# Kernel optimization log

Hardware: AMD Instinct MI355X
Metric: run time of the kernel (lower is better)

The kernel has to match this reference:

```python
import jax, jax.numpy as jnp
import numpy as np

N_NODES = 50000
N_EDGES = 640000
D_IN = 128
D_HID = 128
D_OUT = 128


def setup_inputs() -> dict:
    key = jax.random.key(0)
    ks = jax.random.split(key, 8)
    x = jax.random.normal(ks[0], (N_NODES, D_IN), dtype=jnp.float32)
    edge_index = jax.random.randint(ks[1], (2, N_EDGES), 0, N_NODES, dtype=jnp.int64)
    s1 = 1.0 / np.sqrt(D_IN)
    s2 = 1.0 / np.sqrt(D_HID)
    W1_l = jax.random.uniform(ks[2], (D_IN, D_HID), jnp.float32, -s1, s1)
    W1_r = jax.random.uniform(ks[3], (D_IN, D_HID), jnp.float32, -s1, s1)
    b1 = jnp.zeros((D_HID,), jnp.float32)
    W2_l = jax.random.uniform(ks[4], (D_HID, D_OUT), jnp.float32, -s2, s2)
    W2_r = jax.random.uniform(ks[5], (D_HID, D_OUT), jnp.float32, -s2, s2)
    b2 = jnp.zeros((D_OUT,), jnp.float32)
    return {"x": x, "edge_index": edge_index,
            "W1_l": W1_l, "b1": b1, "W1_r": W1_r,
            "W2_l": W2_l, "b2": b2, "W2_r": W2_r}


def _sage_conv(x, src, dst, W_l, b_l, W_r, n_nodes):
    # mean-aggregate neighbor (source) features onto destinations
    agg = jax.ops.segment_sum(x[src], dst, num_segments=n_nodes)  # [N, d]
    cnt = jax.ops.segment_sum(jnp.ones((src.shape[0],), x.dtype), dst,
                              num_segments=n_nodes)  # [N]
    mean = agg / jnp.maximum(cnt, 1.0)[:, None]
    # PyG SAGEConv: lin_l(aggr) [with bias] + lin_r(x) [root weight, no bias]
    return mean @ W_l + b_l + x @ W_r


def reference(x, edge_index, W1_l, b1, W1_r, W2_l, b2, W2_r):
    src, dst = edge_index[0], edge_index[1]
    n = x.shape[0]
    h = _sage_conv(x, src, dst, W1_l, b1, W1_r, n)
    h = jax.nn.relu(h)
    h = _sage_conv(h, src, dst, W2_l, b2, W2_r, n)
    return h
```

## Files before the change

kernel.cpp:

```cpp
#include <hip/hip_runtime.h>

#define N_NODES 50000
#define N_EDGES 640000
#define D 128

#define SCAN_BLOCK 256
#define SCAN_NBLK ((N_NODES + SCAN_BLOCK - 1) / SCAN_BLOCK)

typedef __attribute__((ext_vector_type(8))) short bf16x8;
typedef __attribute__((ext_vector_type(4))) float f32x4;

__device__ __forceinline__ unsigned short f2bf(float f) {
    union { float f; unsigned u; } v; v.f = f;
    unsigned u = v.u;
    unsigned r = u + 0x7FFFu + ((u >> 16) & 1u);
    return (unsigned short)(r >> 16);
}
__device__ __forceinline__ float bf2f(unsigned short s) {
    union { unsigned u; float f; } v; v.u = ((unsigned)s) << 16; return v.f;
}

__global__ void deg_kernel(const int* __restrict__ dst, int* __restrict__ deg) {
    int e = blockIdx.x * blockDim.x + threadIdx.x;
    if (e < N_EDGES) atomicAdd(&deg[dst[e]], 1);
}

__global__ __launch_bounds__(SCAN_BLOCK) void scan_partial(const int* __restrict__ deg,
                                                           int* __restrict__ partial) {
    __shared__ int sm[SCAN_BLOCK];
    const int t = threadIdx.x;
    const int i = blockIdx.x * SCAN_BLOCK + t;
    sm[t] = (i < N_NODES) ? deg[i] : 0;
    __syncthreads();
#pragma unroll
    for (int off = SCAN_BLOCK / 2; off > 0; off >>= 1) {
        if (t < off) sm[t] += sm[t + off];
        __syncthreads();
    }
    if (t == 0) partial[blockIdx.x] = sm[0];
}

__global__ __launch_bounds__(SCAN_BLOCK) void scan_offsets(const int* __restrict__ partial,
                                                           int* __restrict__ block_off,
                                                           int* __restrict__ row_off) {
    __shared__ int sm[SCAN_BLOCK];
    const int t = threadIdx.x;
    int v = (t < SCAN_NBLK) ? partial[t] : 0;
    sm[t] = v;
    __syncthreads();
    int x = v;
#pragma unroll
    for (int off = 1; off < SCAN_BLOCK; off <<= 1) {
        int y = (t >= off) ? sm[t - off] : 0;
        __syncthreads();
        x += y;
        sm[t] = x;
        __syncthreads();
    }
    if (t < SCAN_NBLK) block_off[t] = x - v;
    if (t == SCAN_BLOCK - 1) row_off[N_NODES] = x;
}

__global__ __launch_bounds__(SCAN_BLOCK) void scan_final(const int* __restrict__ deg,
                                                         const int* __restrict__ block_off,
                                                         int* __restrict__ row_off,
                                                         int* __restrict__ cursor) {
    __shared__ int sm[SCAN_BLOCK];
    const int t = threadIdx.x;
    const int i = blockIdx.x * SCAN_BLOCK + t;
    int v = (i < N_NODES) ? deg[i] : 0;
    sm[t] = v;
    __syncthreads();
    int x = v;
#pragma unroll
    for (int off = 1; off < SCAN_BLOCK; off <<= 1) {
        int y = (t >= off) ? sm[t - off] : 0;
        __syncthreads();
        x += y;
        sm[t] = x;
        __syncthreads();
    }
    int excl = x - v + block_off[blockIdx.x];
    if (i < N_NODES) {
        row_off[i] = excl;
        cursor[i] = excl;
    }
}

__global__ void fill_csr(const int* __restrict__ src, const int* __restrict__ dst,
                         int* __restrict__ cursor, int* __restrict__ csr_src) {
    int e = blockIdx.x * blockDim.x + threadIdx.x;
    if (e < N_EDGES) {
        int pos = atomicAdd(&cursor[dst[e]], 1);
        csr_src[pos] = src[e];
    }
}

__global__ void cvt_and_wt(const float* __restrict__ x,
                           const float* __restrict__ W1l, const float* __restrict__ W1r,
                           const float* __restrict__ W2l, const float* __restrict__ W2r,
                           unsigned short* __restrict__ x_bf,
                           unsigned short* __restrict__ Wt1,
                           unsigned short* __restrict__ Wt2,
                           int* __restrict__ deg) {
    const int b = blockIdx.x;
    const int t = threadIdx.x;
    if (b < 3125) {
        int i = b * 256 + t;
        float4 a = *reinterpret_cast<const float4*>(&x[(size_t)i * 8]);
        float4 c = *reinterpret_cast<const float4*>(&x[(size_t)i * 8 + 4]);
        bf16x8 o;
        o[0] = (short)f2bf(a.x); o[1] = (short)f2bf(a.y);
        o[2] = (short)f2bf(a.z); o[3] = (short)f2bf(a.w);
        o[4] = (short)f2bf(c.x); o[5] = (short)f2bf(c.y);
        o[6] = (short)f2bf(c.z); o[7] = (short)f2bf(c.w);
        *reinterpret_cast<bf16x8*>(&x_bf[(size_t)i * 8]) = o;
    } else if (b < 3381) {
        const bool second = (b >= 3125 + 128);
        const float* Wl = second ? W2l : W1l;
        const float* Wr = second ? W2r : W1r;
        unsigned short* Wt = second ? Wt2 : Wt1;
        int i = (b - (second ? 3253 : 3125)) * 256 + t;
        int c = i >> 8, k = i & 255;
        float v = (k < 128) ? Wl[k * 128 + c] : Wr[(k - 128) * 128 + c];
        Wt[c * 256 + k] = f2bf(v);
    } else {
        int i = (b - 3381) * 256 + t;
        if (i < N_NODES) deg[i] = 0;
    }
}

template <bool RELU, bool OUTBF16>
__global__ __launch_bounds__(512) void sage_fused(
    const unsigned short* __restrict__ Aroot,
    const int* __restrict__ row_off,
    const int* __restrict__ csr_src,
    const unsigned short* __restrict__ Wt,
    const float* __restrict__ bias,
    float* __restrict__ outf,
    unsigned short* __restrict__ outb)
{
    __shared__ bf16x8 ws[4096];
    const int t = threadIdx.x;
    const int w = t >> 6;
    const int l = t & 63;
    const int row0 = blockIdx.x * 128 + w * 16;

    int node = row0 + (l & 15);
    if (node >= N_NODES) node = N_NODES - 1;
    const int k8 = (l >> 4) * 8;

#pragma unroll
    for (int i = 0; i < 8; ++i) {
        int g = i * 512 + t;
        int col = g >> 5;
        int chunk = g & 31;
        ws[col * 32 + (chunk ^ (col & 7))] =
            *reinterpret_cast<const bf16x8*>(&Wt[(size_t)g * 8]);
    }

    const int beg = row_off[node];
    const int end = row_off[node + 1];
    float s[4][8] = {};
    int k = beg;
    for (; k + 1 < end; k += 2) {
        int n0 = csr_src[k];
        int n1 = csr_src[k + 1];
        const unsigned short* b0 = &Aroot[(size_t)n0 * D + k8];
        const unsigned short* b1 = &Aroot[(size_t)n1 * D + k8];
        bf16x8 v0[4], v1[4];
#pragma unroll
        for (int kc = 0; kc < 4; ++kc)
            v0[kc] = *reinterpret_cast<const bf16x8*>(b0 + kc * 32);
#pragma unroll
        for (int kc = 0; kc < 4; ++kc)
            v1[kc] = *reinterpret_cast<const bf16x8*>(b1 + kc * 32);
#pragma unroll
        for (int kc = 0; kc < 4; ++kc)
#pragma unroll
            for (int j = 0; j < 8; ++j)
                s[kc][j] += bf2f((unsigned short)v0[kc][j])
                          + bf2f((unsigned short)v1[kc][j]);
    }
    if (k < end) {
        int n0 = csr_src[k];
        const unsigned short* b0 = &Aroot[(size_t)n0 * D + k8];
#pragma unroll
        for (int kc = 0; kc < 4; ++kc) {
            bf16x8 v0 = *reinterpret_cast<const bf16x8*>(b0 + kc * 32);
#pragma unroll
            for (int j = 0; j < 8; ++j) s[kc][j] += bf2f((unsigned short)v0[j]);
        }
    }

    bf16x8 a[8];
    {
        const float inv = 1.0f / fmaxf((float)(end - beg), 1.0f);
#pragma unroll
        for (int kc = 0; kc < 4; ++kc) {
            bf16x8 o;
#pragma unroll
            for (int j = 0; j < 8; ++j) o[j] = (short)f2bf(s[kc][j] * inv);
            a[kc] = o;
        }
    }
#pragma unroll
    for (int kc = 0; kc < 4; ++kc)
        a[4 + kc] = *reinterpret_cast<const bf16x8*>(
            &Aroot[(size_t)node * D + kc * 32 + k8]);

    __syncthreads();

    f32x4 acc[8] = {};
    const int l15 = l & 15;
    const int kg = l >> 4;
    const int swz = l & 7;
#pragma unroll
    for (int kc = 0; kc < 8; ++kc) {
#pragma unroll
        for (int c = 0; c < 8; ++c) {
            bf16x8 bfr = ws[c * 512 + l15 * 32 + ((kc * 4 + kg) ^ swz)];
            acc[c] = __builtin_amdgcn_mfma_f32_16x16x32_bf16(a[kc], bfr, acc[c], 0, 0, 0);
        }
    }

    const int rbase = row0 + kg * 4;
#pragma unroll
    for (int c = 0; c < 8; ++c) {
        const int col = c * 16 + l15;
        const float b = bias[col];
#pragma unroll
        for (int i = 0; i < 4; ++i) {
            int r = rbase + i;
            if (r < N_NODES) {
                float v = acc[c][i] + b;
                if (RELU) v = fmaxf(v, 0.f);
                if (OUTBF16) outb[(size_t)r * D + col] = f2bf(v);
                else         outf[(size_t)r * D + col] = v;
            }
        }
    }
}

extern "C" void kernel_launch(void* const* d_in, const int* in_sizes, int n_in,
                              void* d_out, int out_size, void* d_ws, size_t ws_size,
                              hipStream_t stream) {
    const float* x   = (const float*)d_in[0];
    const int*   ei  = (const int*)d_in[1];
    const float* W1l = (const float*)d_in[2];
    const float* b1  = (const float*)d_in[3];
    const float* W1r = (const float*)d_in[4];
    const float* W2l = (const float*)d_in[5];
    const float* b2  = (const float*)d_in[6];
    const float* W2r = (const float*)d_in[7];
    float* out = (float*)d_out;

    const int* src = ei;
    const int* dst = ei + N_EDGES;

    int* deg       = (int*)d_ws;
    int* row_off   = deg + 51200;
    int* cursor    = row_off + 51200;
    int* partial   = cursor + 51200;
    int* block_off = partial + 256;
    int* csr_src   = block_off + 256;
    unsigned short* x_bf = (unsigned short*)(csr_src + N_EDGES);
    unsigned short* h_bf = x_bf + (size_t)N_NODES * D;
    unsigned short* Wt1  = h_bf + (size_t)N_NODES * D;
    unsigned short* Wt2  = Wt1 + 128 * 256;

    cvt_and_wt<<<3577, 256, 0, stream>>>(x, W1l, W1r, W2l, W2r, x_bf, Wt1, Wt2, deg);
    deg_kernel<<<(N_EDGES + 255) / 256, 256, 0, stream>>>(dst, deg);
    scan_partial<<<SCAN_NBLK, SCAN_BLOCK, 0, stream>>>(deg, partial);
    scan_offsets<<<1, SCAN_BLOCK, 0, stream>>>(partial, block_off, row_off);
    scan_final<<<SCAN_NBLK, SCAN_BLOCK, 0, stream>>>(deg, block_off, row_off, cursor);
    fill_csr<<<(N_EDGES + 255) / 256, 256, 0, stream>>>(src, dst, cursor, csr_src);

    const int gemm_grid = (N_NODES + 127) / 128;

    sage_fused<true, true><<<gemm_grid, 512, 0, stream>>>(
        x_bf, row_off, csr_src, Wt1, b1, nullptr, h_bf);

    sage_fused<false, false><<<gemm_grid, 512, 0, stream>>>(
        h_bf, row_off, csr_src, Wt2, b2, out, nullptr);
}
```

Measured before the change: 164.0 us.

## Merge scan offset kernel into final scan and halve weight LDS footprint

```diff
diff --git a/kernel.cpp b/kernel.cpp
--- a/kernel.cpp
+++ b/kernel.cpp
@@ -40,12 +40,28 @@
     if (t == 0) partial[blockIdx.x] = sm[0];
 }
 
-__global__ __launch_bounds__(SCAN_BLOCK) void scan_offsets(const int* __restrict__ partial,
-                                                           int* __restrict__ block_off,
-                                                           int* __restrict__ row_off) {
+__global__ __launch_bounds__(SCAN_BLOCK) void scan_final2(const int* __restrict__ deg,
+                                                          const int* __restrict__ partial,
+                                                          int* __restrict__ row_off,
+                                                          int* __restrict__ cursor) {
     __shared__ int sm[SCAN_BLOCK];
     const int t = threadIdx.x;
-    int v = (t < SCAN_NBLK) ? partial[t] : 0;
+    const int b = blockIdx.x;
+
+    int acc = 0;
+    for (int i = t; i < b; i += SCAN_BLOCK) acc += partial[i];
+    sm[t] = acc;
+    __syncthreads();
+#pragma unroll
+    for (int off = SCAN_BLOCK / 2; off > 0; off >>= 1) {
+        if (t < off) sm[t] += sm[t + off];
+        __syncthreads();
+    }
+    const int boff = sm[0];
+    __syncthreads();
+
+    const int i = b * SCAN_BLOCK + t;
+    int v = (i < N_NODES) ? deg[i] : 0;
     sm[t] = v;
     __syncthreads();
     int x = v;
@@ -57,34 +73,12 @@
         sm[t] = x;
         __syncthreads();
     }
-    if (t < SCAN_NBLK) block_off[t] = x - v;
-    if (t == SCAN_BLOCK - 1) row_off[N_NODES] = x;
-}
-
-__global__ __launch_bounds__(SCAN_BLOCK) void scan_final(const int* __restrict__ deg,
-                                                         const int* __restrict__ block_off,
-                                                         int* __restrict__ row_off,
-                                                         int* __restrict__ cursor) {
-    __shared__ int sm[SCAN_BLOCK];
-    const int t = threadIdx.x;
-    const int i = blockIdx.x * SCAN_BLOCK + t;
-    int v = (i < N_NODES) ? deg[i] : 0;
-    sm[t] = v;
-    __syncthreads();
-    int x = v;
-#pragma unroll
-    for (int off = 1; off < SCAN_BLOCK; off <<= 1) {
-        int y = (t >= off) ? sm[t - off] : 0;
-        __syncthreads();
-        x += y;
-        sm[t] = x;
-        __syncthreads();
-    }
-    int excl = x - v + block_off[blockIdx.x];
+    int excl = x - v + boff;
     if (i < N_NODES) {
         row_off[i] = excl;
         cursor[i] = excl;
     }
+    if (b == SCAN_NBLK - 1 && t == SCAN_BLOCK - 1) row_off[N_NODES] = x + boff;
 }
 
 __global__ void fill_csr(const int* __restrict__ src, const int* __restrict__ dst,
@@ -131,7 +125,7 @@
 }
 
 template <bool RELU, bool OUTBF16>
-__global__ __launch_bounds__(512) void sage_fused(
+__global__ __launch_bounds__(512, 8) void sage_fused(
     const unsigned short* __restrict__ Aroot,
     const int* __restrict__ row_off,
     const int* __restrict__ csr_src,
@@ -140,7 +134,7 @@
     float* __restrict__ outf,
     unsigned short* __restrict__ outb)
 {
-    __shared__ bf16x8 ws[4096];
+    __shared__ bf16x8 ws[2048];
     const int t = threadIdx.x;
     const int w = t >> 6;
     const int l = t & 63;
@@ -151,12 +145,12 @@
     const int k8 = (l >> 4) * 8;
 
 #pragma unroll
-    for (int i = 0; i < 8; ++i) {
-        int g = i * 512 + t;
-        int col = g >> 5;
-        int chunk = g & 31;
+    for (int i = 0; i < 4; ++i) {
+        int s = i * 512 + t;
+        int col = s >> 5;
+        int chunk = s & 31;
         ws[col * 32 + (chunk ^ (col & 7))] =
-            *reinterpret_cast<const bf16x8*>(&Wt[(size_t)g * 8]);
+            *reinterpret_cast<const bf16x8*>(&Wt[((size_t)col * 32 + chunk) * 8]);
     }
 
     const int beg = row_off[node];
@@ -215,11 +209,32 @@
     const int l15 = l & 15;
     const int kg = l >> 4;
     const int swz = l & 7;
+
 #pragma unroll
     for (int kc = 0; kc < 8; ++kc) {
 #pragma unroll
-        for (int c = 0; c < 8; ++c) {
+        for (int c = 0; c < 4; ++c) {
             bf16x8 bfr = ws[c * 512 + l15 * 32 + ((kc * 4 + kg) ^ swz)];
+            acc[c] = __builtin_amdgcn_mfma_f32_16x16x32_bf16(a[kc], bfr, acc[c], 0, 0, 0);
+        }
+    }
+    __syncthreads();
+
+#pragma unroll
+    for (int i = 0; i < 4; ++i) {
+        int s2 = i * 512 + t;
+        int col = s2 >> 5;
+        int chunk = s2 & 31;
+        ws[col * 32 + (chunk ^ (col & 7))] =
+            *reinterpret_cast<const bf16x8*>(&Wt[((size_t)(64 + col) * 32 + chunk) * 8]);
+    }
+    __syncthreads();
+
+#pragma unroll
+    for (int kc = 0; kc < 8; ++kc) {
+#pragma unroll
+        for (int c = 4; c < 8; ++c) {
+            bf16x8 bfr = ws[(c - 4) * 512 + l15 * 32 + ((kc * 4 + kg) ^ swz)];
             acc[c] = __builtin_amdgcn_mfma_f32_16x16x32_bf16(a[kc], bfr, acc[c], 0, 0, 0);
         }
     }
@@ -272,8 +287,7 @@
     cvt_and_wt<<<3577, 256, 0, stream>>>(x, W1l, W1r, W2l, W2r, x_bf, Wt1, Wt2, deg);
     deg_kernel<<<(N_EDGES + 255) / 256, 256, 0, stream>>>(dst, deg);
     scan_partial<<<SCAN_NBLK, SCAN_BLOCK, 0, stream>>>(deg, partial);
-    scan_offsets<<<1, SCAN_BLOCK, 0, stream>>>(partial, block_off, row_off);
-    scan_final<<<SCAN_NBLK, SCAN_BLOCK, 0, stream>>>(deg, block_off, row_off, cursor);
+    scan_final2<<<SCAN_NBLK, SCAN_BLOCK, 0, stream>>>(deg, partial, row_off, cursor);
     fill_csr<<<(N_EDGES + 255) / 256, 256, 0, stream>>>(src, dst, cursor, csr_src);
 
     const int gemm_grid = (N_NODES + 127) / 128;
```

Measured after the change: 229.6 us. 1.4x slower.
